# Kernel optimization log

Measured on AMD Instinct MI355X. Metric: run time of the kernel, lower is better.

## Reference

```python
import jax, jax.numpy as jnp
import numpy as np

N = 100000   # active voxels
K = 27       # 3x3x3 kernel offsets
C = 64       # in_channels == out_channels (residual block)
EPS = 1e-5


def setup_inputs() -> dict:
    key = jax.random.key(0)
    ks = jax.random.split(key, 10)
    feats = jax.random.normal(ks[0], (N, C), dtype=jnp.float32)
    # kernel-map: for each voxel, index of the neighbor voxel for each of the 27 offsets
    nbr = jax.random.randint(ks[1], (N, K), 0, N)
    nbr = nbr.at[:, K // 2].set(jnp.arange(N))  # center offset is identity
    w_scale = 1.0 / np.sqrt(K * C)
    W1 = jax.random.normal(ks[2], (K, C, C), dtype=jnp.float32) * w_scale
    b1 = jax.random.normal(ks[3], (C,), dtype=jnp.float32) * 0.01
    g1 = jnp.ones((C,), jnp.float32)
    be1 = jnp.zeros((C,), jnp.float32)
    W2 = jax.random.normal(ks[4], (K, C, C), dtype=jnp.float32) * w_scale
    b2 = jax.random.normal(ks[5], (C,), dtype=jnp.float32) * 0.01
    g2 = jnp.ones((C,), jnp.float32)
    be2 = jnp.zeros((C,), jnp.float32)
    return {"feats": feats, "nbr": nbr, "W1": W1, "b1": b1, "g1": g1, "be1": be1,
            "W2": W2, "b2": b2, "g2": g2, "be2": be2}


def _sparse_conv(f, nbr, W, b):
    # gather neighbor features per kernel offset: [N, K, C]
    g = f[nbr]
    # per-offset matmul and reduce over offsets (gather-matmul-scatter form)
    return jnp.einsum('nkc,kcd->nd', g, W) + b


def _bn(x, gamma, beta):
    # BatchNorm over active voxels (training-mode batch stats, per channel)
    mu = x.mean(axis=0)
    var = x.var(axis=0)
    return (x - mu) * jax.lax.rsqrt(var + EPS) * gamma + beta


def reference(feats, nbr, W1, b1, g1, be1, W2, b2, g2, be2):
    h = jax.nn.relu(_bn(_sparse_conv(feats, nbr, W1, b1), g1, be1))
    h = _bn(_sparse_conv(h, nbr, W2, b2), g2, be2)
    return jax.nn.relu(h + feats)  # residual add + ReLU
```

## Files before the change

kernel.cpp:

```cpp
#include <hip/hip_runtime.h>

#define NCH 64
#define KOFF 27
#define EPSV 1e-5f

typedef __attribute__((ext_vector_type(8))) short  bf16x8;
typedef __attribute__((ext_vector_type(4))) float  f32x4;
typedef __attribute__((ext_vector_type(8))) unsigned short u16x8;

__device__ __forceinline__ unsigned short f2bf(float x) {
    unsigned int u = __float_as_uint(x);
    u += 0x7fffu + ((u >> 16) & 1u);
    return (unsigned short)(u >> 16);
}

__global__ __launch_bounds__(256)
void prep_kernel(const float* __restrict__ feats,
                 const float* __restrict__ W1, const float* __restrict__ W2,
                 unsigned short* __restrict__ fbf,
                 unsigned short* __restrict__ wt1, unsigned short* __restrict__ wt2,
                 float* __restrict__ stat, int total8)
{
    const int b = blockIdx.x;
    if (b == 0) {
        stat[threadIdx.x] = 0.f;
        return;
    }
    if (b <= 108) {
        const float* W = (b <= 54) ? W1 : W2;
        unsigned short* Wt = (b <= 54) ? wt1 : wt2;
        const int t = (b <= 54 ? b - 1 : b - 55) * 256 + threadIdx.x;
        const int l  = t & 63;
        const int ct = (t >> 6) & 3;
        const int s  = (t >> 8) & 1;
        const int k  = t >> 9;
        const int d     = ct * 16 + (l & 15);
        const int cbase = s * 32 + (l >> 4) * 8;
        u16x8 o;
#pragma unroll
        for (int j = 0; j < 8; ++j)
            o[j] = f2bf(W[(size_t)k * 4096 + (size_t)(cbase + j) * 64 + d]);
        reinterpret_cast<u16x8*>(Wt)[t] = o;
        return;
    }
    const int idx = (b - 109) * 256 + threadIdx.x;
    if (idx >= total8) return;
    const float4* xp = reinterpret_cast<const float4*>(feats) + (size_t)idx * 2;
    const float4 a = xp[0], c = xp[1];
    u16x8 o;
    o[0] = f2bf(a.x); o[1] = f2bf(a.y); o[2] = f2bf(a.z); o[3] = f2bf(a.w);
    o[4] = f2bf(c.x); o[5] = f2bf(c.y); o[6] = f2bf(c.z); o[7] = f2bf(c.w);
    reinterpret_cast<u16x8*>(fbf)[idx] = o;
}

__global__ __launch_bounds__(64, 2)
void conv_mfma_kernel(const unsigned short* __restrict__ fin,
                      const int* __restrict__ nbr,
                      const unsigned short* __restrict__ Wt,
                      const float* __restrict__ bias,
                      float* __restrict__ out, float* __restrict__ stat, int N)
{
    __shared__ int s_idx[KOFF * 64 + 64];

    const int lane = threadIdx.x;
    const int n0   = blockIdx.x * 64;
    const int m    = lane & 15;
    const int quad = lane >> 4;

    {
        const int rem  = N - n0;
        const int maxi = (rem < 64 ? rem : 64) * KOFF;
        const int* nb  = nbr + (size_t)n0 * KOFF;
#pragma unroll
        for (int j = 0; j < KOFF; ++j) {
            const int p = j * 64 + lane;
            s_idx[p] = (p < maxi) ? nb[p] : 0;
        }
    }

    f32x4 acc[4][4];
#pragma unroll
    for (int mt = 0; mt < 4; ++mt)
#pragma unroll
        for (int ct = 0; ct < 4; ++ct) acc[mt][ct] = (f32x4){0.f, 0.f, 0.f, 0.f};

    bf16x8 A[2][4][2];
    bf16x8 B[2][2][4];

#define LOADK(k, p)                                                          \
    {                                                                        \
        _Pragma("unroll")                                                    \
        for (int mt = 0; mt < 4; ++mt) {                                     \
            const int r = s_idx[(mt * 16 + m) * KOFF + (k)];                 \
            const unsigned short* fp = fin + (size_t)r * NCH + quad * 8;     \
            A[p][mt][0] = *reinterpret_cast<const bf16x8*>(fp);              \
            A[p][mt][1] = *reinterpret_cast<const bf16x8*>(fp + 32);         \
        }                                                                    \
        const unsigned short* wp = Wt + (size_t)(k) * 4096 + lane * 8;       \
        _Pragma("unroll")                                                    \
        for (int s = 0; s < 2; ++s)                                          \
            _Pragma("unroll")                                                \
            for (int ct = 0; ct < 4; ++ct)                                   \
                B[p][s][ct] =                                                \
                    *reinterpret_cast<const bf16x8*>(wp + (s * 4 + ct) * 512);\
    }

#define DOMFMA(p)                                                            \
    {                                                                        \
        _Pragma("unroll")                                                    \
        for (int mt = 0; mt < 4; ++mt)                                       \
            _Pragma("unroll")                                                \
            for (int s = 0; s < 2; ++s)                                      \
                _Pragma("unroll")                                            \
                for (int ct = 0; ct < 4; ++ct)                               \
                    acc[mt][ct] = __builtin_amdgcn_mfma_f32_16x16x32_bf16(   \
                        A[p][mt][s], B[p][s][ct], acc[mt][ct], 0, 0, 0);     \
    }

    LOADK(0, 0);
#pragma unroll 1
    for (int k = 0; k < KOFF - 1; k += 2) {
        LOADK(k + 1, 1);
        DOMFMA(0);
        LOADK(k + 2, 0);
        DOMFMA(1);
    }
    DOMFMA(0);

#pragma unroll
    for (int ct = 0; ct < 4; ++ct) {
        const int ch = ct * 16 + m;
        const float bv = bias[ch];
        float s = 0.f, q = 0.f;
#pragma unroll
        for (int mt = 0; mt < 4; ++mt) {
#pragma unroll
            for (int r = 0; r < 4; ++r) {
                const int vox = n0 + mt * 16 + quad * 4 + r;
                if (vox < N) {
                    const float v = acc[mt][ct][r] + bv;
                    out[(size_t)vox * NCH + ch] = v;
                    s += v;
                    q += v * v;
                }
            }
        }
        s += __shfl_xor(s, 16, 64);
        s += __shfl_xor(s, 32, 64);
        q += __shfl_xor(q, 16, 64);
        q += __shfl_xor(q, 32, 64);
        if (quad == 0) {
            atomicAdd(&stat[ch], s);
            atomicAdd(&stat[64 + ch], q);
        }
    }
#undef LOADK
#undef DOMFMA
}

__global__ __launch_bounds__(256)
void bn_relu_bf16_kernel(const float* __restrict__ x, const float* __restrict__ sums,
                         const float* __restrict__ gmm, const float* __restrict__ bet,
                         float invN, unsigned short* __restrict__ y, int total8)
{
    const int idx = blockIdx.x * 256 + threadIdx.x;
    if (idx >= total8) return;
    const int c0 = (idx & 7) * 8;
    const float4* xp = reinterpret_cast<const float4*>(x) + (size_t)idx * 2;
    const float4 a = xp[0], b = xp[1];
    float v[8] = {a.x, a.y, a.z, a.w, b.x, b.y, b.z, b.w};
    u16x8 o;
#pragma unroll
    for (int i = 0; i < 8; ++i) {
        const int c = c0 + i;
        const float mu  = sums[c] * invN;
        const float var = sums[64 + c] * invN - mu * mu;
        const float rs  = rsqrtf(var + EPSV);
        const float sc  = gmm[c] * rs;
        const float sh  = bet[c] - mu * sc;
        o[i] = f2bf(fmaxf(fmaf(v[i], sc, sh), 0.f));
    }
    reinterpret_cast<u16x8*>(y)[idx] = o;
}

__global__ __launch_bounds__(256)
void bn_res_relu_kernel(float* __restrict__ x, const float* __restrict__ feats,
                        const float* __restrict__ sums, const float* __restrict__ gmm,
                        const float* __restrict__ bet, float invN, int total4)
{
    const int idx = blockIdx.x * blockDim.x + threadIdx.x;
    if (idx >= total4) return;
    float4 v = reinterpret_cast<float4*>(x)[idx];
    const float4 f = reinterpret_cast<const float4*>(feats)[idx];
    const int c0 = (idx & 15) * 4;
    float sc[4], sh[4];
#pragma unroll
    for (int i = 0; i < 4; ++i) {
        const int c = c0 + i;
        const float mu  = sums[c] * invN;
        const float var = sums[64 + c] * invN - mu * mu;
        const float rs  = rsqrtf(var + EPSV);
        sc[i] = gmm[c] * rs;
        sh[i] = bet[c] - mu * sc[i];
    }
    v.x = fmaxf(fmaf(v.x, sc[0], sh[0]) + f.x, 0.f);
    v.y = fmaxf(fmaf(v.y, sc[1], sh[1]) + f.y, 0.f);
    v.z = fmaxf(fmaf(v.z, sc[2], sh[2]) + f.z, 0.f);
    v.w = fmaxf(fmaf(v.w, sc[3], sh[3]) + f.w, 0.f);
    reinterpret_cast<float4*>(x)[idx] = v;
}

extern "C" void kernel_launch(void* const* d_in, const int* in_sizes, int n_in,
                              void* d_out, int out_size, void* d_ws, size_t ws_size,
                              hipStream_t stream)
{
    const float* feats = (const float*)d_in[0];
    const int*   nbr   = (const int*)d_in[1];
    const float* W1    = (const float*)d_in[2];
    const float* b1    = (const float*)d_in[3];
    const float* g1    = (const float*)d_in[4];
    const float* be1   = (const float*)d_in[5];
    const float* W2    = (const float*)d_in[6];
    const float* b2    = (const float*)d_in[7];
    const float* g2    = (const float*)d_in[8];
    const float* be2   = (const float*)d_in[9];
    float* out = (float*)d_out;

    const int N  = in_sizes[0] / NCH;
    const int NC = N * NCH;
    const float invN = 1.0f / (float)N;

    float*          h0   = (float*)d_ws;
    unsigned short* fbf  = (unsigned short*)(h0 + NC);
    unsigned short* hbf  = fbf + NC;
    unsigned short* wt1  = hbf + NC;
    unsigned short* wt2  = wt1 + KOFF * 4096;
    float*          stat = (float*)(wt2 + KOFF * 4096);

    const int total8   = NC / 8;
    const int castGrid = (total8 + 255) / 256;
    const int prepGrid = 1 + 108 + castGrid;
    const int convGrid = (N + 63) / 64;

    prep_kernel<<<prepGrid, 256, 0, stream>>>(feats, W1, W2, fbf, wt1, wt2,
                                              stat, total8);
    conv_mfma_kernel<<<convGrid, 64, 0, stream>>>(fbf, nbr, wt1, b1, h0, stat, N);
    bn_relu_bf16_kernel<<<castGrid, 256, 0, stream>>>(h0, stat, g1, be1, invN,
                                                      hbf, total8);
    conv_mfma_kernel<<<convGrid, 64, 0, stream>>>(hbf, nbr, wt2, b2, out,
                                                  stat + 128, N);
    bn_res_relu_kernel<<<(NC / 4 + 255) / 256, 256, 0, stream>>>(
        out, feats, stat + 128, g2, be2, invN, NC / 4);
}
```

Baseline: 322.8 us.

## Restructure sparse conv to 4-wave blocks with asm-pipelined loads and bf16 intermediate

Each conv block now holds four wavefronts, each handling 32 voxels instead of one wave handling 64. The gather and weight loads are issued as inline-asm global loads, double-buffered with explicit vmcnt waits and a fully unrolled K loop, so memory latency can overlap the MFMAs. Neighbor indices are pre-scaled to byte offsets in shared memory. The first conv now writes its pre-BN output as bf16, which halves intermediate traffic at some precision cost. Weights are re-read per wave with fewer voxels per wave, so weight traffic per voxel doubles.

```diff
diff --git a/kernel.cpp b/kernel.cpp
--- a/kernel.cpp
+++ b/kernel.cpp
@@ -53,79 +53,113 @@
     reinterpret_cast<u16x8*>(fbf)[idx] = o;
 }
 
-__global__ __launch_bounds__(64, 2)
+template <typename OUT_T>
+__global__ __launch_bounds__(256, 3)
 void conv_mfma_kernel(const unsigned short* __restrict__ fin,
                       const int* __restrict__ nbr,
                       const unsigned short* __restrict__ Wt,
                       const float* __restrict__ bias,
-                      float* __restrict__ out, float* __restrict__ stat, int N)
-{
-    __shared__ int s_idx[KOFF * 64 + 64];
-
-    const int lane = threadIdx.x;
-    const int n0   = blockIdx.x * 64;
+                      OUT_T* __restrict__ out, float* __restrict__ stat, int N)
+{
+    __shared__ int s_idx[4 * 32 * KOFF];
+
+    const int t    = threadIdx.x;
+    const int lane = t & 63;
+    const int w    = t >> 6;
+    const int n0   = (blockIdx.x * 4 + w) * 32;
     const int m    = lane & 15;
     const int quad = lane >> 4;
+    int* sw = s_idx + w * (32 * KOFF);
 
     {
-        const int rem  = N - n0;
-        const int maxi = (rem < 64 ? rem : 64) * KOFF;
+        int rem = N - n0;
+        rem = rem < 0 ? 0 : (rem > 32 ? 32 : rem);
+        const int maxi = rem * KOFF;
         const int* nb  = nbr + (size_t)n0 * KOFF;
-#pragma unroll
-        for (int j = 0; j < KOFF; ++j) {
-            const int p = j * 64 + lane;
-            s_idx[p] = (p < maxi) ? nb[p] : 0;
-        }
-    }
-
-    f32x4 acc[4][4];
-#pragma unroll
-    for (int mt = 0; mt < 4; ++mt)
+        for (int p = lane; p < 32 * KOFF; p += 64)
+            sw[p] = ((p < maxi) ? nb[p] : 0) * (NCH * 2);
+    }
+
+    const char* finB = (const char*)fin;
+    const char* WtB  = (const char*)Wt;
+
+    f32x4 acc[2][4];
+#pragma unroll
+    for (int mt = 0; mt < 2; ++mt)
 #pragma unroll
         for (int ct = 0; ct < 4; ++ct) acc[mt][ct] = (f32x4){0.f, 0.f, 0.f, 0.f};
 
-    bf16x8 A[2][4][2];
+    bf16x8 A[2][2][2];
     bf16x8 B[2][2][4];
 
-#define LOADK(k, p)                                                          \
-    {                                                                        \
-        _Pragma("unroll")                                                    \
-        for (int mt = 0; mt < 4; ++mt) {                                     \
-            const int r = s_idx[(mt * 16 + m) * KOFF + (k)];                 \
-            const unsigned short* fp = fin + (size_t)r * NCH + quad * 8;     \
-            A[p][mt][0] = *reinterpret_cast<const bf16x8*>(fp);              \
-            A[p][mt][1] = *reinterpret_cast<const bf16x8*>(fp + 32);         \
-        }                                                                    \
-        const unsigned short* wp = Wt + (size_t)(k) * 4096 + lane * 8;       \
-        _Pragma("unroll")                                                    \
-        for (int s = 0; s < 2; ++s)                                          \
-            _Pragma("unroll")                                                \
-            for (int ct = 0; ct < 4; ++ct)                                   \
-                B[p][s][ct] =                                                \
-                    *reinterpret_cast<const bf16x8*>(wp + (s * 4 + ct) * 512);\
-    }
-
-#define DOMFMA(p)                                                            \
-    {                                                                        \
-        _Pragma("unroll")                                                    \
-        for (int mt = 0; mt < 4; ++mt)                                       \
-            _Pragma("unroll")                                                \
-            for (int s = 0; s < 2; ++s)                                      \
-                _Pragma("unroll")                                            \
-                for (int ct = 0; ct < 4; ++ct)                               \
-                    acc[mt][ct] = __builtin_amdgcn_mfma_f32_16x16x32_bf16(   \
-                        A[p][mt][s], B[p][s][ct], acc[mt][ct], 0, 0, 0);     \
-    }
-
-    LOADK(0, 0);
-#pragma unroll 1
-    for (int k = 0; k < KOFF - 1; k += 2) {
-        LOADK(k + 1, 1);
-        DOMFMA(0);
-        LOADK(k + 2, 0);
-        DOMFMA(1);
-    }
-    DOMFMA(0);
+#define LOADK(kk, p)                                                          \
+    {                                                                         \
+        const char* fp0 = finB + sw[(0 * 16 + m) * KOFF + (kk)] + quad * 16;  \
+        const char* fp1 = finB + sw[(1 * 16 + m) * KOFF + (kk)] + quad * 16;  \
+        asm volatile("global_load_dwordx4 %0, %1, off"                        \
+                     : "=v"(A[p][0][0]) : "v"(fp0));                          \
+        asm volatile("global_load_dwordx4 %0, %1, off offset:64"              \
+                     : "=v"(A[p][0][1]) : "v"(fp0));                          \
+        asm volatile("global_load_dwordx4 %0, %1, off"                        \
+                     : "=v"(A[p][1][0]) : "v"(fp1));                          \
+        asm volatile("global_load_dwordx4 %0, %1, off offset:64"              \
+                     : "=v"(A[p][1][1]) : "v"(fp1));                          \
+        const char* wp = WtB + (kk)*8192 + lane * 16;                         \
+        asm volatile("global_load_dwordx4 %0, %1, off"                        \
+                     : "=v"(B[p][0][0]) : "v"(wp));                           \
+        asm volatile("global_load_dwordx4 %0, %1, off offset:1024"            \
+                     : "=v"(B[p][0][1]) : "v"(wp));                           \
+        asm volatile("global_load_dwordx4 %0, %1, off offset:2048"            \
+                     : "=v"(B[p][0][2]) : "v"(wp));                           \
+        asm volatile("global_load_dwordx4 %0, %1, off offset:3072"            \
+                     : "=v"(B[p][0][3]) : "v"(wp));                           \
+        const char* wq = wp + 4096;                                           \
+        asm volatile("global_load_dwordx4 %0, %1, off"                        \
+                     : "=v"(B[p][1][0]) : "v"(wq));                           \
+        asm volatile("global_load_dwordx4 %0, %1, off offset:1024"            \
+                     : "=v"(B[p][1][1]) : "v"(wq));                           \
+        asm volatile("global_load_dwordx4 %0, %1, off offset:2048"            \
+                     : "=v"(B[p][1][2]) : "v"(wq));                           \
+        asm volatile("global_load_dwordx4 %0, %1, off offset:3072"            \
+                     : "=v"(B[p][1][3]) : "v"(wq));                           \
+    }
+
+#define WAITDEP(p, VMSTR)                                                     \
+    asm volatile("s_waitcnt vmcnt(" VMSTR ")"                                 \
+                 : "+v"(A[p][0][0]), "+v"(A[p][0][1]),                        \
+                   "+v"(A[p][1][0]), "+v"(A[p][1][1]),                        \
+                   "+v"(B[p][0][0]), "+v"(B[p][0][1]),                        \
+                   "+v"(B[p][0][2]), "+v"(B[p][0][3]),                        \
+                   "+v"(B[p][1][0]), "+v"(B[p][1][1]),                        \
+                   "+v"(B[p][1][2]), "+v"(B[p][1][3]) :: "memory");
+
+#define DOMFMA(p)                                                             \
+    {                                                                         \
+        _Pragma("unroll")                                                     \
+        for (int mt = 0; mt < 2; ++mt)                                        \
+            _Pragma("unroll")                                                 \
+            for (int sf = 0; sf < 2; ++sf)                                    \
+                _Pragma("unroll")                                             \
+                for (int ct = 0; ct < 4; ++ct)                                \
+                    acc[mt][ct] = __builtin_amdgcn_mfma_f32_16x16x32_bf16(    \
+                        A[p][mt][sf], B[p][sf][ct], acc[mt][ct], 0, 0, 0);    \
+    }
+
+#define STEPK(kk)                                                             \
+    WAITDEP((kk) & 1, "12") DOMFMA((kk) & 1) LOADK((kk) + 2, (kk) & 1)
+
+    LOADK(0, 0) LOADK(1, 1)
+    STEPK(0)  STEPK(1)  STEPK(2)  STEPK(3)  STEPK(4)
+    STEPK(5)  STEPK(6)  STEPK(7)  STEPK(8)  STEPK(9)
+    STEPK(10) STEPK(11) STEPK(12) STEPK(13) STEPK(14)
+    STEPK(15) STEPK(16) STEPK(17) STEPK(18) STEPK(19)
+    STEPK(20) STEPK(21) STEPK(22) STEPK(23) STEPK(24)
+    WAITDEP(1, "12") DOMFMA(1)
+    WAITDEP(0, "0")  DOMFMA(0)
+#undef LOADK
+#undef WAITDEP
+#undef DOMFMA
+#undef STEPK
 
 #pragma unroll
     for (int ct = 0; ct < 4; ++ct) {
@@ -133,13 +167,16 @@
         const float bv = bias[ch];
         float s = 0.f, q = 0.f;
 #pragma unroll
-        for (int mt = 0; mt < 4; ++mt) {
+        for (int mt = 0; mt < 2; ++mt) {
 #pragma unroll
             for (int r = 0; r < 4; ++r) {
                 const int vox = n0 + mt * 16 + quad * 4 + r;
                 if (vox < N) {
                     const float v = acc[mt][ct][r] + bv;
-                    out[(size_t)vox * NCH + ch] = v;
+                    if constexpr (__is_same(OUT_T, unsigned short))
+                        out[(size_t)vox * NCH + ch] = f2bf(v);
+                    else
+                        out[(size_t)vox * NCH + ch] = v;
                     s += v;
                     q += v * v;
                 }
@@ -154,21 +191,18 @@
             atomicAdd(&stat[64 + ch], q);
         }
     }
-#undef LOADK
-#undef DOMFMA
 }
 
 __global__ __launch_bounds__(256)
-void bn_relu_bf16_kernel(const float* __restrict__ x, const float* __restrict__ sums,
+void bn_relu_bf16_kernel(const unsigned short* __restrict__ x,
+                         const float* __restrict__ sums,
                          const float* __restrict__ gmm, const float* __restrict__ bet,
                          float invN, unsigned short* __restrict__ y, int total8)
 {
     const int idx = blockIdx.x * 256 + threadIdx.x;
     if (idx >= total8) return;
     const int c0 = (idx & 7) * 8;
-    const float4* xp = reinterpret_cast<const float4*>(x) + (size_t)idx * 2;
-    const float4 a = xp[0], b = xp[1];
-    float v[8] = {a.x, a.y, a.z, a.w, b.x, b.y, b.z, b.w};
+    const u16x8 a = reinterpret_cast<const u16x8*>(x)[idx];
     u16x8 o;
 #pragma unroll
     for (int i = 0; i < 8; ++i) {
@@ -178,7 +212,8 @@
         const float rs  = rsqrtf(var + EPSV);
         const float sc  = gmm[c] * rs;
         const float sh  = bet[c] - mu * sc;
-        o[i] = f2bf(fmaxf(fmaf(v[i], sc, sh), 0.f));
+        const float v   = __uint_as_float((unsigned)a[i] << 16);
+        o[i] = f2bf(fmaxf(fmaf(v, sc, sh), 0.f));
     }
     reinterpret_cast<u16x8*>(y)[idx] = o;
 }
@@ -230,9 +265,9 @@
     const int NC = N * NCH;
     const float invN = 1.0f / (float)N;
 
-    float*          h0   = (float*)d_ws;
-    unsigned short* fbf  = (unsigned short*)(h0 + NC);
-    unsigned short* hbf  = fbf + NC;
+    unsigned short* fbf  = (unsigned short*)d_ws;
+    unsigned short* hpre = fbf + NC;
+    unsigned short* hbf  = hpre + NC;
     unsigned short* wt1  = hbf + NC;
     unsigned short* wt2  = wt1 + KOFF * 4096;
     float*          stat = (float*)(wt2 + KOFF * 4096);
@@ -240,15 +275,16 @@
     const int total8   = NC / 8;
     const int castGrid = (total8 + 255) / 256;
     const int prepGrid = 1 + 108 + castGrid;
-    const int convGrid = (N + 63) / 64;
+    const int convGrid = (N + 127) / 128;
 
     prep_kernel<<<prepGrid, 256, 0, stream>>>(feats, W1, W2, fbf, wt1, wt2,
                                               stat, total8);
-    conv_mfma_kernel<<<convGrid, 64, 0, stream>>>(fbf, nbr, wt1, b1, h0, stat, N);
-    bn_relu_bf16_kernel<<<castGrid, 256, 0, stream>>>(h0, stat, g1, be1, invN,
+    conv_mfma_kernel<unsigned short><<<convGrid, 256, 0, stream>>>(
+        fbf, nbr, wt1, b1, hpre, stat, N);
+    bn_relu_bf16_kernel<<<castGrid, 256, 0, stream>>>(hpre, stat, g1, be1, invN,
                                                       hbf, total8);
-    conv_mfma_kernel<<<convGrid, 64, 0, stream>>>(hbf, nbr, wt2, b2, out,
-                                                  stat + 128, N);
+    conv_mfma_kernel<float><<<convGrid, 256, 0, stream>>>(
+        hbf, nbr, wt2, b2, out, stat + 128, N);
     bn_res_relu_kernel<<<(NC / 4 + 255) / 256, 256, 0, stream>>>(
         out, feats, stat + 128, g2, be2, invN, NC / 4);
 }
```

New measurement: 366.4 us. +13.5%, slower.
